# Kernel tuning notes

Hardware: AMD Instinct MI355X
Metric: run time of the kernel (lower is better)

## Reference

```python
import jax, jax.numpy as jnp
import numpy as np

N, E, F_IN, HID, EDIM, OUT = 50000, 800000, 128, 128, 32, 1
NEG_SLOPE = 0.2


def setup_inputs() -> dict:
    key = jax.random.key(0)
    ks = jax.random.split(key, 24)
    sc = 0.05
    d = {}
    d["x"] = jax.random.normal(ks[0], (N, F_IN), jnp.float32)
    d["src"] = jax.random.randint(ks[1], (E,), 0, N)
    d["dst"] = jax.random.randint(ks[2], (E,), 0, N)
    d["edge_attr"] = jax.random.normal(ks[3], (E, EDIM), jnp.float32)
    # conv1 params (GATConv(F_IN -> HID, edge_dim=EDIM), heads=1)
    d["W1"] = jax.random.normal(ks[4], (F_IN, HID), jnp.float32) * sc
    d["We1"] = jax.random.normal(ks[5], (EDIM, HID), jnp.float32) * sc
    d["as1"] = jax.random.normal(ks[6], (HID,), jnp.float32) * sc
    d["ad1"] = jax.random.normal(ks[7], (HID,), jnp.float32) * sc
    d["ae1"] = jax.random.normal(ks[8], (HID,), jnp.float32) * sc
    d["b1"] = jnp.zeros((HID,), jnp.float32)
    # conv2 params (GATConv(HID -> HID, edge_dim=EDIM))
    d["W2"] = jax.random.normal(ks[9], (HID, HID), jnp.float32) * sc
    d["We2"] = jax.random.normal(ks[10], (EDIM, HID), jnp.float32) * sc
    d["as2"] = jax.random.normal(ks[11], (HID,), jnp.float32) * sc
    d["ad2"] = jax.random.normal(ks[12], (HID,), jnp.float32) * sc
    d["ae2"] = jax.random.normal(ks[13], (HID,), jnp.float32) * sc
    d["b2"] = jnp.zeros((HID,), jnp.float32)
    # final linear
    d["Wl"] = jax.random.normal(ks[14], (HID, OUT), jnp.float32) * sc
    d["bl"] = jnp.zeros((OUT,), jnp.float32)
    return d


def _gat_conv(x, src, dst, e_attr, W, We, a_s, a_d, a_e, b):
    # x: [N, Fin], src/dst: [Et], e_attr: [Et, EDIM]
    h = x @ W                      # [N, C]
    ee = e_attr @ We               # [Et, C]
    alpha = h @ a_s                # per-node source logit [N]
    beta = h @ a_d                 # per-node dest logit   [N]
    logit = alpha[src] + beta[dst] + ee @ a_e          # [Et]
    logit = jax.nn.leaky_relu(logit, NEG_SLOPE)
    # segment softmax over destination node
    m = jax.ops.segment_max(logit, dst, num_segments=N)
    ex = jnp.exp(logit - m[dst])
    s = jax.ops.segment_sum(ex, dst, num_segments=N)
    w = ex / (s[dst] + 1e-16)                          # [Et]
    out = jax.ops.segment_sum(h[src] * w[:, None], dst, num_segments=N)
    return out + b


def reference(x, src, dst, edge_attr, W1, We1, as1, ad1, ae1, b1,
              W2, We2, as2, ad2, ae2, b2, Wl, bl):
    # add_self_loops=True with fill_value='mean' (PyG GATConv default)
    loop = jnp.arange(N, dtype=src.dtype)
    src2 = jnp.concatenate([src, loop])
    dst2 = jnp.concatenate([dst, loop])
    mean_ea = jnp.mean(edge_attr, axis=0)
    ea2 = jnp.concatenate([edge_attr, jnp.broadcast_to(mean_ea, (N, EDIM))], axis=0)
    h = _gat_conv(x, src2, dst2, ea2, W1, We1, as1, ad1, ae1, b1)
    h = jax.nn.relu(h)                 # dropout is identity in eval mode
    h = _gat_conv(h, src2, dst2, ea2, W2, We2, as2, ad2, ae2, b2)
    out = h @ Wl + bl
    return jax.nn.relu(out)            # [N, 1]
```

## Files before the change

kernel.cpp:

```cpp
#include <hip/hip_runtime.h>
#include <math.h>

#define N_NODES 50000
#define N_EDGES 800000
#define HIDDEN  128
#define EDIM    32
#define NEG     0.2f

typedef __attribute__((ext_vector_type(8))) short bshort8;
typedef __attribute__((ext_vector_type(4))) float f32x4;

__device__ __forceinline__ unsigned short f2bf(float f) {
    unsigned u = __builtin_bit_cast(unsigned, f);
    return (unsigned short)((u + 0x7FFFu + ((u >> 16) & 1u)) >> 16);
}
__device__ __forceinline__ float bf2f(unsigned short b) {
    unsigned u = ((unsigned)b) << 16;
    return __builtin_bit_cast(float, u);
}

#define TILES_M (N_NODES / 16)
#define GEMM_BLOCKS ((TILES_M + 3) / 4)
#define EB (N_EDGES / 256)
#define SCAN_BLOCKS ((N_NODES + 255) / 256)

__device__ __forceinline__ void pack_w_body(int idx, const float* __restrict__ W,
                                            unsigned short* __restrict__ whp,
                                            unsigned short* __restrict__ wlp) {
    int e  = idx & 7;
    int l  = (idx >> 3) & 63;
    int kc = (idx >> 9) & 3;
    int ct = (idx >> 11);
    int k   = kc * 32 + ((l >> 4) << 3) + e;
    int col = ct * 16 + (l & 15);
    float w = W[k * HIDDEN + col];
    unsigned short hb = f2bf(w);
    whp[idx] = hb;
    wlp[idx] = f2bf(w - bf2f(hb));
}

__device__ __forceinline__ void gemm_body(int tile, int t,
                                          const float* __restrict__ x,
                                          const unsigned short* __restrict__ wh,
                                          const unsigned short* __restrict__ wl,
                                          const float* __restrict__ a_s,
                                          const float* __restrict__ a_d,
                                          float* __restrict__ h,
                                          float* __restrict__ alpha,
                                          float* __restrict__ beta) {
    int l    = t & 63;
    int row0 = tile * 16;
    int arow = l & 15;
    int kg   = l >> 4;
    bshort8 ah[4], al[4];
    const float* xr = x + (size_t)(row0 + arow) * HIDDEN + (kg << 3);
#pragma unroll
    for (int kc = 0; kc < 4; kc++) {
        float4 f0 = *(const float4*)(xr + kc * 32);
        float4 f1 = *(const float4*)(xr + kc * 32 + 4);
        float fv[8] = {f0.x, f0.y, f0.z, f0.w, f1.x, f1.y, f1.z, f1.w};
#pragma unroll
        for (int e = 0; e < 8; e++) {
            unsigned short hb = f2bf(fv[e]);
            ah[kc][e] = (short)hb;
            al[kc][e] = (short)f2bf(fv[e] - bf2f(hb));
        }
    }
    float pal[4] = {0.f, 0.f, 0.f, 0.f};
    float pbe[4] = {0.f, 0.f, 0.f, 0.f};
#pragma unroll
    for (int ct = 0; ct < 8; ct++) {
        f32x4 acc = {0.f, 0.f, 0.f, 0.f};
#pragma unroll
        for (int kc = 0; kc < 4; kc++) {
            int fo = (((ct * 4 + kc) * 64) + l) << 3;
            bshort8 bh = *(const bshort8*)(wh + fo);
            bshort8 bl = *(const bshort8*)(wl + fo);
            acc = __builtin_amdgcn_mfma_f32_16x16x32_bf16(ah[kc], bh, acc, 0, 0, 0);
            acc = __builtin_amdgcn_mfma_f32_16x16x32_bf16(al[kc], bh, acc, 0, 0, 0);
            acc = __builtin_amdgcn_mfma_f32_16x16x32_bf16(ah[kc], bl, acc, 0, 0, 0);
        }
        int col = ct * 16 + arow;
        float a_sc = a_s[col], a_dc = a_d[col];
#pragma unroll
        for (int j = 0; j < 4; j++) {
            h[(size_t)(row0 + kg * 4 + j) * HIDDEN + col] = acc[j];
            pal[j] += acc[j] * a_sc;
            pbe[j] += acc[j] * a_dc;
        }
    }
#pragma unroll
    for (int m = 1; m < 16; m <<= 1) {
#pragma unroll
        for (int j = 0; j < 4; j++) {
            pal[j] += __shfl_xor(pal[j], m, 64);
            pbe[j] += __shfl_xor(pbe[j], m, 64);
        }
    }
    if (arow == 0) {
#pragma unroll
        for (int j = 0; j < 4; j++) {
            alpha[row0 + kg * 4 + j] = pal[j];
            beta[row0 + kg * 4 + j]  = pbe[j];
        }
    }
}

__global__ void __launch_bounds__(256)
fused_prep_kernel(const int* __restrict__ dst, int* __restrict__ count,
                  int* __restrict__ rank,
                  const float* __restrict__ W1, unsigned short* __restrict__ whp1,
                  unsigned short* __restrict__ wlp1,
                  const float* __restrict__ We1, const float* __restrict__ ae1,
                  const float* __restrict__ We2, const float* __restrict__ ae2,
                  const float* __restrict__ W2,
                  const float* __restrict__ as2, const float* __restrict__ ad2,
                  const float* __restrict__ b2, const float* __restrict__ Wlin,
                  const float* __restrict__ bl, float* __restrict__ consts) {
    int b = blockIdx.x, t = threadIdx.x;
    if (b < EB) {
        int e = b * 256 + t;
        rank[e] = atomicAdd(&count[dst[e]], 1);
    } else if (b < EB + 64) {
        pack_w_body((b - EB) * 256 + t, W1, whp1, wlp1);
    } else if (b == EB + 64) {
        if (t < 32) {
            float acc = 0.f;
            for (int k = 0; k < HIDDEN; k++) acc += We1[t * HIDDEN + k] * ae1[k];
            consts[t] = acc;
        } else if (t < 64) {
            int j = t - 32;
            float acc = 0.f;
            for (int k = 0; k < HIDDEN; k++) acc += We2[j * HIDDEN + k] * ae2[k];
            consts[32 + j] = acc;
        } else if (t < 128) {
            int k = t - 64;
            float p = b2[k] * Wlin[k] + b2[k + 64] * Wlin[k + 64];
            for (int off = 32; off > 0; off >>= 1) p += __shfl_down(p, off, 64);
            if (t == 64) consts[64] = p + bl[0];
        }
    } else {
        if (t < HIDDEN) {
            const float* wr = W2 + (size_t)t * HIDDEN;
            float su = 0.f, sa = 0.f, sb = 0.f;
            for (int k = 0; k < HIDDEN; k++) {
                float w = wr[k];
                su += w * Wlin[k];
                sa += w * as2[k];
                sb += w * ad2[k];
            }
            consts[128 + t] = su;
            consts[256 + t] = sa;
            consts[384 + t] = sb;
        }
    }
}

__global__ void scan1_kernel(const int* __restrict__ count,
                             int* __restrict__ off_work, int* __restrict__ blocksum) {
    __shared__ int sh[256];
    int t = threadIdx.x;
    int idx = blockIdx.x * 256 + t;
    int v = (idx < N_NODES) ? count[idx] : 0;
    sh[t] = v;
    __syncthreads();
    for (int off = 1; off < 256; off <<= 1) {
        int u = (t >= off) ? sh[t - off] : 0;
        __syncthreads();
        sh[t] += u;
        __syncthreads();
    }
    if (idx < N_NODES) off_work[idx] = sh[t] - v;
    if (t == 255) blocksum[blockIdx.x] = sh[255];
}
__global__ void scan2_kernel(int* __restrict__ blocksum, int* __restrict__ blockoff) {
    __shared__ int sh[256];
    int t = threadIdx.x;
    int v = (t < SCAN_BLOCKS) ? blocksum[t] : 0;
    sh[t] = v;
    __syncthreads();
    for (int off = 1; off < 256; off <<= 1) {
        int u = (t >= off) ? sh[t - off] : 0;
        __syncthreads();
        sh[t] += u;
        __syncthreads();
    }
    if (t < SCAN_BLOCKS) blockoff[t] = sh[t] - v;
}

__global__ void __launch_bounds__(256)
fused_scatter_gemm_kernel(const int* __restrict__ src, const int* __restrict__ dst,
                          const int* __restrict__ rank,
                          const float* __restrict__ ea,
                          const float* __restrict__ consts,
                          const int* __restrict__ off_work,
                          const int* __restrict__ blockoff,
                          float4* __restrict__ erec, float* __restrict__ part,
                          const float* __restrict__ x,
                          const unsigned short* __restrict__ wh,
                          const unsigned short* __restrict__ wl,
                          const float* __restrict__ a_s, const float* __restrict__ a_d,
                          float* __restrict__ h, float* __restrict__ alpha,
                          float* __restrict__ beta) {
    __shared__ float cs[64];
    int b = blockIdx.x, t = threadIdx.x;
    bool is_gemm = ((b & 3) == 3) && ((b >> 2) < GEMM_BLOCKS);
    if (is_gemm) {
        int tile = (b >> 2) * 4 + (t >> 6);
        if (tile < TILES_M)
            gemm_body(tile, t, x, wh, wl, a_s, a_d, h, alpha, beta);
        return;
    }
    int sid = b - min((b + 1) >> 2, GEMM_BLOCKS);
    if (t < 64) cs[t] = consts[t];
    __syncthreads();
    int e = sid * 256 + t;
    const float4* ep = (const float4*)(ea + (size_t)e * EDIM);
    float d1 = 0.f, d2 = 0.f;
#pragma unroll
    for (int i = 0; i < 8; i++) {
        float4 v = ep[i];
        d1 += v.x * cs[4 * i] + v.y * cs[4 * i + 1] + v.z * cs[4 * i + 2] + v.w * cs[4 * i + 3];
        d2 += v.x * cs[32 + 4 * i] + v.y * cs[32 + 4 * i + 1] + v.z * cs[32 + 4 * i + 2] + v.w * cs[32 + 4 * i + 3];
    }
    int d = dst[e];
    int pos = off_work[d] + blockoff[d >> 8] + rank[e];
    erec[pos] = make_float4(d1, d2, __int_as_float(src[e]), 0.f);
    float s1 = d1, s2 = d2;
    for (int off = 32; off > 0; off >>= 1) {
        s1 += __shfl_down(s1, off, 64);
        s2 += __shfl_down(s2, off, 64);
    }
    if ((t & 63) == 0) {
        int slot = (sid & 63) * 16;
        atomicAdd(&part[slot], s1);
        atomicAdd(&part[slot + 1], s2);
    }
}

__global__ void __launch_bounds__(256)
agg1_kernel(const int* __restrict__ off_work, const int* __restrict__ blockoff,
            const int* __restrict__ count, const float4* __restrict__ erec,
            const float* __restrict__ h,
            const float* __restrict__ alpha, const float* __restrict__ beta,
            const float* __restrict__ b, const float* __restrict__ part,
            const float* __restrict__ consts,
            float* __restrict__ beta2, float2* __restrict__ pg) {
    int t = threadIdx.x;
    int l = t & 63;
    int i = blockIdx.x * 4 + (t >> 6);
    float ps = part[l * 16];
#pragma unroll
    for (int m = 32; m > 0; m >>= 1) ps += __shfl_xor(ps, m, 64);
    float selfc = ps * (1.f / (float)N_EDGES);
    int start = off_work[i] + blockoff[i >> 8];
    int end   = start + count[i];
    float beta_i = beta[i];
    float2 acc = make_float2(0.f, 0.f);
    float wsum = 0.f;
    for (int cb = start; cb < end; cb += 64) {
        int n = min(64, end - cb);
        int sp = 0; float wt = 0.f;
        if (l < n) {
            float4 rec = erec[cb + l];
            sp = __float_as_int(rec.z);
            float lg = alpha[sp] + beta_i + rec.x;
            lg = lg > 0.f ? lg : NEG * lg;
            wt = expf(lg);
        }
        int j = 0;
        for (; j + 8 <= n; j += 8) {
            float w8[8]; int s8[8]; float2 h8[8];
#pragma unroll
            for (int q = 0; q < 8; q++) {
                w8[q] = __shfl(wt, j + q, 64);
                s8[q] = __shfl(sp, j + q, 64);
            }
#pragma unroll
            for (int q = 0; q < 8; q++)
                h8[q] = ((const float2*)(h + (size_t)s8[q] * HIDDEN))[l];
#pragma unroll
            for (int q = 0; q < 8; q++) {
                acc.x += w8[q] * h8[q].x;
                acc.y += w8[q] * h8[q].y;
                wsum  += w8[q];
            }
        }
        for (; j + 4 <= n; j += 4) {
            float w4[4]; int s4[4]; float2 h4[4];
#pragma unroll
            for (int q = 0; q < 4; q++) {
                w4[q] = __shfl(wt, j + q, 64);
                s4[q] = __shfl(sp, j + q, 64);
            }
#pragma unroll
            for (int q = 0; q < 4; q++)
                h4[q] = ((const float2*)(h + (size_t)s4[q] * HIDDEN))[l];
#pragma unroll
            for (int q = 0; q < 4; q++) {
                acc.x += w4[q] * h4[q].x;
                acc.y += w4[q] * h4[q].y;
                wsum  += w4[q];
            }
        }
        for (; j < n; j++) {
            float w = __shfl(wt, j, 64);
            int   sj = __shfl(sp, j, 64);
            float2 hv = ((const float2*)(h + (size_t)sj * HIDDEN))[l];
            acc.x += w * hv.x;
            acc.y += w * hv.y;
            wsum  += w;
        }
    }
    float lg = alpha[i] + beta_i + selfc;
    lg = lg > 0.f ? lg : NEG * lg;
    float exi = expf(lg);
    float denom = wsum + exi + 1e-16f;
    float2 hv = ((const float2*)(h + (size_t)i * HIDDEN))[l];
    float2 bb = ((const float2*)b)[l];
    float bx = fmaxf((acc.x + exi * hv.x) / denom + bb.x, 0.f);
    float by = fmaxf((acc.y + exi * hv.y) / denom + bb.y, 0.f);
    int c0 = 2 * l, c1 = 2 * l + 1;
    float pa2 = bx * consts[256 + c0] + by * consts[256 + c1];
    float pb2 = bx * consts[384 + c0] + by * consts[384 + c1];
    float pgv = bx * consts[128 + c0] + by * consts[128 + c1];
#pragma unroll
    for (int m = 32; m > 0; m >>= 1) {
        pa2 += __shfl_xor(pa2, m, 64);
        pb2 += __shfl_xor(pb2, m, 64);
        pgv += __shfl_xor(pgv, m, 64);
    }
    if (l == 0) {
        beta2[i] = pb2;
        pg[i] = make_float2(pa2, pgv);
    }
}

__global__ void __launch_bounds__(256)
agg2_lite_kernel(const int* __restrict__ off_work, const int* __restrict__ blockoff,
                 const int* __restrict__ count, const float4* __restrict__ erec,
                 const float2* __restrict__ pg, const float* __restrict__ beta2,
                 const float* __restrict__ part, const float* __restrict__ consts,
                 float* __restrict__ out) {
    int t = threadIdx.x, l = t & 63;
    int i = blockIdx.x * 4 + (t >> 6);
    float ps = part[l * 16 + 1];
#pragma unroll
    for (int m = 32; m > 0; m >>= 1) ps += __shfl_xor(ps, m, 64);
    float selfc = ps * (1.f / (float)N_EDGES);
    int start = off_work[i] + blockoff[i >> 8];
    int end   = start + count[i];
    float beta_i = beta2[i];
    float wsum = 0.f, gsum = 0.f;
    for (int e = start + l; e < end; e += 64) {
        float4 rec = erec[e];
        int sp = __float_as_int(rec.z);
        float2 ag = pg[sp];
        float lg = ag.x + beta_i + rec.y;
        lg = lg > 0.f ? lg : NEG * lg;
        float w = expf(lg);
        wsum += w;
        gsum += w * ag.y;
    }
    for (int m = 32; m > 0; m >>= 1) {
        wsum += __shfl_xor(wsum, m, 64);
        gsum += __shfl_xor(gsum, m, 64);
    }
    if (l == 0) {
        float2 agi = pg[i];
        float lg = agi.x + beta_i + selfc;
        lg = lg > 0.f ? lg : NEG * lg;
        float exi = expf(lg);
        float denom = wsum + exi + 1e-16f;
        out[i] = fmaxf((gsum + exi * agi.y) / denom + consts[64], 0.f);
    }
}

extern "C" void kernel_launch(void* const* d_in, const int* in_sizes, int n_in,
                              void* d_out, int out_size, void* d_ws, size_t ws_size,
                              hipStream_t stream) {
    const float* x   = (const float*)d_in[0];
    const int*   src = (const int*)  d_in[1];
    const int*   dst = (const int*)  d_in[2];
    const float* ea  = (const float*)d_in[3];
    const float* W1  = (const float*)d_in[4];
    const float* We1 = (const float*)d_in[5];
    const float* as1 = (const float*)d_in[6];
    const float* ad1 = (const float*)d_in[7];
    const float* ae1 = (const float*)d_in[8];
    const float* b1  = (const float*)d_in[9];
    const float* W2  = (const float*)d_in[10];
    const float* We2 = (const float*)d_in[11];
    const float* as2 = (const float*)d_in[12];
    const float* ad2 = (const float*)d_in[13];
    const float* ae2 = (const float*)d_in[14];
    const float* b2  = (const float*)d_in[15];
    const float* Wl  = (const float*)d_in[16];
    const float* bl  = (const float*)d_in[17];
    float* out = (float*)d_out;

    float* ws      = (float*)d_ws;
    float* A       = ws;
    float4* erec   = (float4*)(A + (size_t)N_NODES * HIDDEN);
    unsigned short* whp1 = (unsigned short*)(erec + N_EDGES);
    unsigned short* wlp1 = whp1 + 16384;
    float* alpha1  = (float*)(wlp1 + 16384);
    float* beta1   = alpha1 + N_NODES;
    float* beta2   = beta1 + N_NODES;
    float2* pg     = (float2*)(beta2 + N_NODES);
    float* consts  = (float*)(pg + N_NODES);
    float* part    = consts + 512;
    int* count     = (int*)(part + 64 * 16);
    int* off_work  = count + N_NODES;
    int* blocksum  = off_work + N_NODES;
    int* blockoff  = blocksum + SCAN_BLOCKS;
    int* rank      = blockoff + SCAN_BLOCKS;

    hipMemsetAsync(count, 0, N_NODES * sizeof(int), stream);
    hipMemsetAsync(part, 0, 64 * 16 * sizeof(float), stream);
    fused_prep_kernel<<<EB + 66, 256, 0, stream>>>(dst, count, rank,
                                                   W1, whp1, wlp1,
                                                   We1, ae1, We2, ae2,
                                                   W2, as2, ad2, b2, Wl, bl,
                                                   consts);
    scan1_kernel<<<SCAN_BLOCKS, 256, 0, stream>>>(count, off_work, blocksum);
    scan2_kernel<<<1, 256, 0, stream>>>(blocksum, blockoff);

    fused_scatter_gemm_kernel<<<EB + GEMM_BLOCKS, 256, 0, stream>>>(
        src, dst, rank, ea, consts, off_work, blockoff, erec, part,
        x, whp1, wlp1, as1, ad1, A, alpha1, beta1);

    agg1_kernel<<<N_NODES / 4, 256, 0, stream>>>(off_work, blockoff, count, erec,
                                                 A, alpha1, beta1, b1, part,
                                                 consts, beta2, pg);

    agg2_lite_kernel<<<N_NODES / 4, 256, 0, stream>>>(off_work, blockoff, count,
                                                      erec, pg, beta2, part,
                                                      consts, out);
}
```

Before: 187.2 us.

## Compute edge logits in prep pass and scatter only edge indices via permutation

Moves the edge-attribute projection and self-loop mean accumulation into the prep kernel, which now writes a compact per-edge record (two bf16 logit terms plus the source index) in original edge order. The scatter kernel now writes only a 4-byte edge-index permutation into CSR order instead of a 16-byte record. A tiny extra kernel computes the We·ae constants beforehand. The aggregation kernels gain an extra indirection (permutation, then a random record read), and the edge logit terms are rounded to bf16, which slightly reduces precision.

```diff
diff --git a/kernel.cpp b/kernel.cpp
--- a/kernel.cpp
+++ b/kernel.cpp
@@ -107,8 +107,10 @@
 }
 
 __global__ void __launch_bounds__(256)
-fused_prep_kernel(const int* __restrict__ dst, int* __restrict__ count,
-                  int* __restrict__ rank,
+fused_prep_kernel(const int* __restrict__ src, const int* __restrict__ dst,
+                  const float* __restrict__ ea,
+                  int* __restrict__ count, int* __restrict__ rank,
+                  uint2* __restrict__ rec, float* __restrict__ part,
                   const float* __restrict__ W1, unsigned short* __restrict__ whp1,
                   unsigned short* __restrict__ wlp1,
                   const float* __restrict__ We1, const float* __restrict__ ae1,
@@ -119,8 +121,33 @@
                   const float* __restrict__ bl, float* __restrict__ consts) {
     int b = blockIdx.x, t = threadIdx.x;
     if (b < EB) {
+        __shared__ float cs[64];
+        if (t < 64) cs[t] = consts[t];
+        __syncthreads();
         int e = b * 256 + t;
+        const float4* ep = (const float4*)(ea + (size_t)e * EDIM);
+        float d1 = 0.f, d2 = 0.f;
+#pragma unroll
+        for (int i = 0; i < 8; i++) {
+            float4 v = ep[i];
+            d1 += v.x * cs[4 * i] + v.y * cs[4 * i + 1] + v.z * cs[4 * i + 2] + v.w * cs[4 * i + 3];
+            d2 += v.x * cs[32 + 4 * i] + v.y * cs[32 + 4 * i + 1] + v.z * cs[32 + 4 * i + 2] + v.w * cs[32 + 4 * i + 3];
+        }
+        uint2 r;
+        r.x = ((unsigned)f2bf(d1) << 16) | (unsigned)f2bf(d2);
+        r.y = (unsigned)src[e];
+        rec[e] = r;
         rank[e] = atomicAdd(&count[dst[e]], 1);
+        float s1 = d1, s2 = d2;
+        for (int off = 32; off > 0; off >>= 1) {
+            s1 += __shfl_down(s1, off, 64);
+            s2 += __shfl_down(s2, off, 64);
+        }
+        if ((t & 63) == 0) {
+            int slot = (b & 63) * 16;
+            atomicAdd(&part[slot], s1);
+            atomicAdd(&part[slot + 1], s2);
+        }
     } else if (b < EB + 64) {
         pack_w_body((b - EB) * 256 + t, W1, whp1, wlp1);
     } else if (b == EB + 64) {
@@ -156,6 +183,22 @@
     }
 }
 
+__global__ void ce_kernel(const float* __restrict__ We1, const float* __restrict__ ae1,
+                          const float* __restrict__ We2, const float* __restrict__ ae2,
+                          float* __restrict__ consts) {
+    int t = threadIdx.x;
+    if (t < 32) {
+        float acc = 0.f;
+        for (int k = 0; k < HIDDEN; k++) acc += We1[t * HIDDEN + k] * ae1[k];
+        consts[t] = acc;
+    } else if (t < 64) {
+        int j = t - 32;
+        float acc = 0.f;
+        for (int k = 0; k < HIDDEN; k++) acc += We2[j * HIDDEN + k] * ae2[k];
+        consts[32 + j] = acc;
+    }
+}
+
 __global__ void scan1_kernel(const int* __restrict__ count,
                              int* __restrict__ off_work, int* __restrict__ blocksum) {
     __shared__ int sh[256];
@@ -189,20 +232,16 @@
 }
 
 __global__ void __launch_bounds__(256)
-fused_scatter_gemm_kernel(const int* __restrict__ src, const int* __restrict__ dst,
-                          const int* __restrict__ rank,
-                          const float* __restrict__ ea,
-                          const float* __restrict__ consts,
-                          const int* __restrict__ off_work,
-                          const int* __restrict__ blockoff,
-                          float4* __restrict__ erec, float* __restrict__ part,
-                          const float* __restrict__ x,
-                          const unsigned short* __restrict__ wh,
-                          const unsigned short* __restrict__ wl,
-                          const float* __restrict__ a_s, const float* __restrict__ a_d,
-                          float* __restrict__ h, float* __restrict__ alpha,
-                          float* __restrict__ beta) {
-    __shared__ float cs[64];
+fused_einv_gemm_kernel(const int* __restrict__ dst, const int* __restrict__ rank,
+                       const int* __restrict__ off_work,
+                       const int* __restrict__ blockoff,
+                       int* __restrict__ einv,
+                       const float* __restrict__ x,
+                       const unsigned short* __restrict__ wh,
+                       const unsigned short* __restrict__ wl,
+                       const float* __restrict__ a_s, const float* __restrict__ a_d,
+                       float* __restrict__ h, float* __restrict__ alpha,
+                       float* __restrict__ beta) {
     int b = blockIdx.x, t = threadIdx.x;
     bool is_gemm = ((b & 3) == 3) && ((b >> 2) < GEMM_BLOCKS);
     if (is_gemm) {
@@ -212,35 +251,16 @@
         return;
     }
     int sid = b - min((b + 1) >> 2, GEMM_BLOCKS);
-    if (t < 64) cs[t] = consts[t];
-    __syncthreads();
     int e = sid * 256 + t;
-    const float4* ep = (const float4*)(ea + (size_t)e * EDIM);
-    float d1 = 0.f, d2 = 0.f;
-#pragma unroll
-    for (int i = 0; i < 8; i++) {
-        float4 v = ep[i];
-        d1 += v.x * cs[4 * i] + v.y * cs[4 * i + 1] + v.z * cs[4 * i + 2] + v.w * cs[4 * i + 3];
-        d2 += v.x * cs[32 + 4 * i] + v.y * cs[32 + 4 * i + 1] + v.z * cs[32 + 4 * i + 2] + v.w * cs[32 + 4 * i + 3];
-    }
     int d = dst[e];
     int pos = off_work[d] + blockoff[d >> 8] + rank[e];
-    erec[pos] = make_float4(d1, d2, __int_as_float(src[e]), 0.f);
-    float s1 = d1, s2 = d2;
-    for (int off = 32; off > 0; off >>= 1) {
-        s1 += __shfl_down(s1, off, 64);
-        s2 += __shfl_down(s2, off, 64);
-    }
-    if ((t & 63) == 0) {
-        int slot = (sid & 63) * 16;
-        atomicAdd(&part[slot], s1);
-        atomicAdd(&part[slot + 1], s2);
-    }
+    einv[pos] = e;
 }
 
 __global__ void __launch_bounds__(256)
 agg1_kernel(const int* __restrict__ off_work, const int* __restrict__ blockoff,
-            const int* __restrict__ count, const float4* __restrict__ erec,
+            const int* __restrict__ count, const int* __restrict__ einv,
+            const uint2* __restrict__ rec,
             const float* __restrict__ h,
             const float* __restrict__ alpha, const float* __restrict__ beta,
             const float* __restrict__ b, const float* __restrict__ part,
@@ -262,9 +282,11 @@
         int n = min(64, end - cb);
         int sp = 0; float wt = 0.f;
         if (l < n) {
-            float4 rec = erec[cb + l];
-            sp = __float_as_int(rec.z);
-            float lg = alpha[sp] + beta_i + rec.x;
+            int e = einv[cb + l];
+            uint2 r = rec[e];
+            sp = (int)r.y;
+            float d1 = bf2f((unsigned short)(r.x >> 16));
+            float lg = alpha[sp] + beta_i + d1;
             lg = lg > 0.f ? lg : NEG * lg;
             wt = expf(lg);
         }
@@ -338,7 +360,8 @@
 
 __global__ void __launch_bounds__(256)
 agg2_lite_kernel(const int* __restrict__ off_work, const int* __restrict__ blockoff,
-                 const int* __restrict__ count, const float4* __restrict__ erec,
+                 const int* __restrict__ count, const int* __restrict__ einv,
+                 const uint2* __restrict__ rec,
                  const float2* __restrict__ pg, const float* __restrict__ beta2,
                  const float* __restrict__ part, const float* __restrict__ consts,
                  float* __restrict__ out) {
@@ -352,11 +375,13 @@
     int end   = start + count[i];
     float beta_i = beta2[i];
     float wsum = 0.f, gsum = 0.f;
-    for (int e = start + l; e < end; e += 64) {
-        float4 rec = erec[e];
-        int sp = __float_as_int(rec.z);
+    for (int p = start + l; p < end; p += 64) {
+        int e = einv[p];
+        uint2 r = rec[e];
+        int sp = (int)r.y;
+        float d2 = bf2f((unsigned short)(r.x & 0xFFFFu));
         float2 ag = pg[sp];
-        float lg = ag.x + beta_i + rec.y;
+        float lg = ag.x + beta_i + d2;
         lg = lg > 0.f ? lg : NEG * lg;
         float w = expf(lg);
         wsum += w;
@@ -401,8 +426,8 @@
 
     float* ws      = (float*)d_ws;
     float* A       = ws;
-    float4* erec   = (float4*)(A + (size_t)N_NODES * HIDDEN);
-    unsigned short* whp1 = (unsigned short*)(erec + N_EDGES);
+    uint2* rec     = (uint2*)(A + (size_t)N_NODES * HIDDEN);
+    unsigned short* whp1 = (unsigned short*)(rec + N_EDGES);
     unsigned short* wlp1 = whp1 + 16384;
     float* alpha1  = (float*)(wlp1 + 16384);
     float* beta1   = alpha1 + N_NODES;
@@ -415,10 +440,13 @@
     int* blocksum  = off_work + N_NODES;
     int* blockoff  = blocksum + SCAN_BLOCKS;
     int* rank      = blockoff + SCAN_BLOCKS;
+    int* einv      = rank + N_EDGES;
 
     hipMemsetAsync(count, 0, N_NODES * sizeof(int), stream);
     hipMemsetAsync(part, 0, 64 * 16 * sizeof(float), stream);
-    fused_prep_kernel<<<EB + 66, 256, 0, stream>>>(dst, count, rank,
+    ce_kernel<<<1, 64, 0, stream>>>(We1, ae1, We2, ae2, consts);
+    fused_prep_kernel<<<EB + 66, 256, 0, stream>>>(src, dst, ea, count, rank,
+                                                   rec, part,
                                                    W1, whp1, wlp1,
                                                    We1, ae1, We2, ae2,
                                                    W2, as2, ad2, b2, Wl, bl,
@@ -426,15 +454,16 @@
     scan1_kernel<<<SCAN_BLOCKS, 256, 0, stream>>>(count, off_work, blocksum);
     scan2_kernel<<<1, 256, 0, stream>>>(blocksum, blockoff);
 
-    fused_scatter_gemm_kernel<<<EB + GEMM_BLOCKS, 256, 0, stream>>>(
-        src, dst, rank, ea, consts, off_work, blockoff, erec, part,
+    fused_einv_gemm_kernel<<<EB + GEMM_BLOCKS, 256, 0, stream>>>(
+        dst, rank, off_work, blockoff, einv,
         x, whp1, wlp1, as1, ad1, A, alpha1, beta1);
 
-    agg1_kernel<<<N_NODES / 4, 256, 0, stream>>>(off_work, blockoff, count, erec,
+    agg1_kernel<<<N_NODES / 4, 256, 0, stream>>>(off_work, blockoff, count,
+                                                 einv, rec,
                                                  A, alpha1, beta1, b1, part,
                                                  consts, beta2, pg);
 
     agg2_lite_kernel<<<N_NODES / 4, 256, 0, stream>>>(off_work, blockoff, count,
-                                                      erec, pg, beta2, part,
+                                                      einv, rec, pg, beta2, part,
                                                       consts, out);
 }
```

Result: slower. 214.8 us (+14.7%).
